# Kernel optimization log

Hardware: AMD Instinct MI355X
Metric: run time of the kernel (lower is better)

The kernel has to match this reference:

```python
import jax, jax.numpy as jnp
import numpy as np

B, T, C = 4, 1024, 1024
H = 16
DH = C // H  # 64


def setup_inputs() -> dict:
    key = jax.random.key(0)
    ks = jax.random.split(key, 10)
    s = 0.02
    return {
        "x": jax.random.normal(ks[0], (B, T, C), dtype=jnp.float32),
        "Wq": jax.random.normal(ks[1], (C, C), dtype=jnp.float32) * s,
        "bq": jnp.zeros((C,), dtype=jnp.float32),
        "Wk": jax.random.normal(ks[2], (C, C), dtype=jnp.float32) * s,
        "bk": jnp.zeros((C,), dtype=jnp.float32),
        "Wv": jax.random.normal(ks[3], (C, C), dtype=jnp.float32) * s,
        "bv": jnp.zeros((C,), dtype=jnp.float32),
        "Wp": jax.random.normal(ks[4], (C, C), dtype=jnp.float32) * s,
        "bp": jnp.zeros((C,), dtype=jnp.float32),
    }


def reference(x, Wq, bq, Wk, bk, Wv, bv, Wp, bp):
    b, t, c = x.shape
    # QKV projections, split into heads: [b, H, t, DH]
    def heads(y):
        return y.reshape(b, t, H, DH).transpose(0, 2, 1, 3)
    q = heads(x @ Wq + bq)
    k = heads(x @ Wk + bk)
    v = heads(x @ Wv + bv)
    # Causal attention. Original masks with -inf BEFORE scaling; -inf*scale is
    # still -inf, so mask-then-scale == scale-then-mask.
    scores = jnp.einsum("bhqd,bhkd->bhqk", q, k) * (DH ** -0.5)
    causal = jnp.tril(jnp.ones((t, t), dtype=bool))
    scores = jnp.where(causal, scores, -jnp.inf)
    attn = jax.nn.softmax(scores, axis=-1)  # dropout p=0.0 -> identity
    ctx = jnp.einsum("bhqk,bhkd->bhqd", attn, v)
    ctx = ctx.transpose(0, 2, 1, 3).reshape(b, t, c)
    return ctx @ Wp + bp
```

## Files before the change

kernel.cpp:

```cpp
#include <hip/hip_runtime.h>


typedef unsigned short ushort_t;
typedef __attribute__((ext_vector_type(8))) __bf16 bf16x8;
typedef __attribute__((ext_vector_type(8))) unsigned short us8;
typedef __attribute__((ext_vector_type(4))) unsigned short us4;
typedef __attribute__((ext_vector_type(4))) float f32x4;

#define AS1 __attribute__((address_space(1)))
#define AS3 __attribute__((address_space(3)))

#define QSCALE 0.18033688011112042f

__device__ __forceinline__ ushort_t f2bf(float f) {
  unsigned int u = __float_as_uint(f);
  u += 0x7fffu + ((u >> 16) & 1u);
  return (ushort_t)(u >> 16);
}

__device__ __forceinline__ ushort_t f2bf_hw(float f) {
  union { __bf16 b; ushort_t u; } cv;
  cv.b = (__bf16)f;
  return cv.u;
}


__global__ void cvt_fused_kernel(const float* __restrict__ x,
                                 const float* __restrict__ Wq, const float* __restrict__ Wk,
                                 const float* __restrict__ Wv, const float* __restrict__ Wp,
                                 ushort_t* __restrict__ XB,
                                 ushort_t* __restrict__ WQKVT, ushort_t* __restrict__ WPT) {
  const int tid = threadIdx.x;
  if (blockIdx.x < 4096) {
    const int i = blockIdx.x * 256 + tid;
    const float4 v = reinterpret_cast<const float4*>(x)[i];
    us4 o;
    o.x = f2bf(v.x); o.y = f2bf(v.y); o.z = f2bf(v.z); o.w = f2bf(v.w);
    reinterpret_cast<us4*>(XB)[i] = o;
    return;
  }
  __shared__ float t[32][33];
  const int tt = blockIdx.x - 4096;
  const int z = tt >> 10;
  const int tile = tt & 1023;
  const int n0 = (tile & 31) * 32, k0 = (tile >> 5) * 32;
  const float* W = (z == 0) ? Wq : (z == 1) ? Wk : (z == 2) ? Wv : Wp;
  ushort_t* Wt = (z == 3) ? WPT : (WQKVT + ((size_t)z << 20));
  const float wscale = (z == 0) ? QSCALE : 1.0f;
  const int tx = tid & 31, ty = tid >> 5;
#pragma unroll
  for (int i = ty; i < 32; i += 8)
    t[i][tx] = W[(size_t)(k0 + i) * 1024 + n0 + tx];
  __syncthreads();
#pragma unroll
  for (int i = ty; i < 32; i += 8)
    Wt[(size_t)(n0 + i) * 1024 + k0 + tx] = f2bf(t[tx][i] * wscale);
}


__global__ __launch_bounds__(256, 3) void gemm_qkv128_kernel(
    const ushort_t* __restrict__ A, const ushort_t* __restrict__ Bt,
    const float* __restrict__ bq, const float* __restrict__ bk,
    const float* __restrict__ bv, ushort_t* __restrict__ QKVB,
    ushort_t* __restrict__ VT) {
  __shared__ ushort_t As[128 * 64];
  __shared__ ushort_t Bs[128 * 64];
  const int tid = threadIdx.x;
  const int wave = tid >> 6, lane = tid & 63;
  const int lgrp = lane >> 4, lmod = lane & 15;
  const int wr = wave >> 1, wc = wave & 1;
  const int swz = (blockIdx.x & 7) * 96 + (blockIdx.x >> 3);
  const int rowt = swz / 24, colt = swz % 24;
  const int row0 = rowt * 128, col0 = colt * 128;
  const bool isV = (colt >= 16);

  const int sslot = (tid & 7) ^ ((tid >> 3) & 7);
  const int srow = tid >> 3;

  auto stage = [&](int t) {
    const ushort_t* Asrc = A + (size_t)row0 * 1024 + t * 64 + sslot * 8;
    const ushort_t* Bsrc = Bt + (size_t)col0 * 1024 + t * 64 + sslot * 8;
#pragma unroll
    for (int i = 0; i < 4; ++i) {
      __builtin_amdgcn_global_load_lds(
          (AS1 void*)(Asrc + (size_t)(i * 32 + srow) * 1024),
          (AS3 void*)(As + (i * 256 + wave * 64) * 8), 16, 0, 0);
      __builtin_amdgcn_global_load_lds(
          (AS1 void*)(Bsrc + (size_t)(i * 32 + srow) * 1024),
          (AS3 void*)(Bs + (i * 256 + wave * 64) * 8), 16, 0, 0);
    }
  };

  f32x4 acc[4][4] = {};
  const int xm = lmod & 7;

  for (int t = 0; t < 16; ++t) {
    stage(t);
    asm volatile("s_waitcnt vmcnt(0)" ::: "memory");
    __builtin_amdgcn_s_barrier();

    bf16x8 af[4][2], bfr[4][2];
#pragma unroll
    for (int mi = 0; mi < 4; ++mi)
#pragma unroll
      for (int ks = 0; ks < 2; ++ks)
        af[mi][ks] = *reinterpret_cast<const bf16x8*>(
            &As[(wr * 64 + mi * 16 + lmod) * 64 + (((ks << 2) | lgrp) ^ xm) * 8]);
#pragma unroll
    for (int ni = 0; ni < 4; ++ni)
#pragma unroll
      for (int ks = 0; ks < 2; ++ks)
        bfr[ni][ks] = *reinterpret_cast<const bf16x8*>(
            &Bs[(wc * 64 + ni * 16 + lmod) * 64 + (((ks << 2) | lgrp) ^ xm) * 8]);

    __builtin_amdgcn_s_setprio(1);
#pragma unroll
    for (int mi = 0; mi < 4; ++mi)
#pragma unroll
      for (int ni = 0; ni < 4; ++ni)
#pragma unroll
        for (int ks = 0; ks < 2; ++ks)
          acc[mi][ni] = __builtin_amdgcn_mfma_f32_16x16x32_bf16(
              af[mi][ks], bfr[ni][ks], acc[mi][ni], 0, 0, 0);
    __builtin_amdgcn_s_setprio(0);
    __builtin_amdgcn_s_barrier();
  }

  if (!isV) {
    const float* bsel = (col0 < 1024) ? bq : bk;
    const float bsc = (col0 < 1024) ? QSCALE : 1.0f;
    float bvv[4];
#pragma unroll
    for (int ni = 0; ni < 4; ++ni)
      bvv[ni] = bsel[(col0 & 1023) + wc * 64 + ni * 16 + lmod] * bsc;
#pragma unroll
    for (int mi = 0; mi < 4; ++mi) {
#pragma unroll
      for (int ni = 0; ni < 4; ++ni) {
        const int col = col0 + wc * 64 + ni * 16 + lmod;
#pragma unroll
        for (int r = 0; r < 4; ++r) {
          const int row = row0 + wr * 64 + mi * 16 + lgrp * 4 + r;
          QKVB[(size_t)row * 3072 + col] = f2bf(acc[mi][ni][r] + bvv[ni]);
        }
      }
    }
  } else {
    float bvv[4];
#pragma unroll
    for (int ni = 0; ni < 4; ++ni)
      bvv[ni] = bv[(col0 - 2048) + wc * 64 + ni * 16 + lmod];
#pragma unroll
    for (int mi = 0; mi < 4; ++mi) {
#pragma unroll
      for (int ni = 0; ni < 4; ++ni) {
        const int hd = (col0 - 2048) + wc * 64 + ni * 16 + lmod;
        const int R = row0 + wr * 64 + mi * 16 + lgrp * 4;
        const int bb = R >> 10, tl = R & 1023;
        us4 o;
#pragma unroll
        for (int r = 0; r < 4; ++r) o[r] = f2bf(acc[mi][ni][r] + bvv[ni]);
        *reinterpret_cast<us4*>(VT + ((size_t)(bb * 16 + (hd >> 6)) * 64 + (hd & 63)) * 1024 + tl) = o;
      }
    }
  }
}


__global__ __launch_bounds__(256, 2) void gemm_proj_kernel(
    const ushort_t* __restrict__ A, const ushort_t* __restrict__ Bt,
    const float* __restrict__ bias, float* __restrict__ Cout) {
  __shared__ ushort_t As[64 * 64];
  __shared__ ushort_t Bs[128 * 64];
  const int tid = threadIdx.x;
  const int wave = tid >> 6, lane = tid & 63;
  const int lgrp = lane >> 4, lmod = lane & 15;
  const int wr = wave >> 1, wc = wave & 1;
  const int swz = (blockIdx.x & 7) * 64 + (blockIdx.x >> 3);
  const int row0 = (swz >> 3) * 64, col0 = (swz & 7) * 128;

  const int sslot = (tid & 7) ^ ((tid >> 3) & 7);
  const int srow = tid >> 3;

  auto stage = [&](int t) {
    const ushort_t* Asrc = A + (size_t)row0 * 1024 + t * 64 + sslot * 8;
    const ushort_t* Bsrc = Bt + (size_t)col0 * 1024 + t * 64 + sslot * 8;
#pragma unroll
    for (int i = 0; i < 2; ++i)
      __builtin_amdgcn_global_load_lds(
          (AS1 void*)(Asrc + (size_t)(i * 32 + srow) * 1024),
          (AS3 void*)(As + (i * 256 + wave * 64) * 8), 16, 0, 0);
#pragma unroll
    for (int i = 0; i < 4; ++i)
      __builtin_amdgcn_global_load_lds(
          (AS1 void*)(Bsrc + (size_t)(i * 32 + srow) * 1024),
          (AS3 void*)(Bs + (i * 256 + wave * 64) * 8), 16, 0, 0);
  };

  f32x4 acc[2][4] = {};
  const int xm = lmod & 7;

  for (int t = 0; t < 16; ++t) {
    stage(t);
    asm volatile("s_waitcnt vmcnt(0)" ::: "memory");
    __builtin_amdgcn_s_barrier();

    bf16x8 af[2][2], bfr[4][2];
#pragma unroll
    for (int mi = 0; mi < 2; ++mi)
#pragma unroll
      for (int ks = 0; ks < 2; ++ks)
        af[mi][ks] = *reinterpret_cast<const bf16x8*>(
            &As[(wr * 32 + mi * 16 + lmod) * 64 + (((ks << 2) | lgrp) ^ xm) * 8]);
#pragma unroll
    for (int ni = 0; ni < 4; ++ni)
#pragma unroll
      for (int ks = 0; ks < 2; ++ks)
        bfr[ni][ks] = *reinterpret_cast<const bf16x8*>(
            &Bs[(wc * 64 + ni * 16 + lmod) * 64 + (((ks << 2) | lgrp) ^ xm) * 8]);

    __builtin_amdgcn_s_setprio(1);
#pragma unroll
    for (int mi = 0; mi < 2; ++mi)
#pragma unroll
      for (int ni = 0; ni < 4; ++ni)
#pragma unroll
        for (int ks = 0; ks < 2; ++ks)
          acc[mi][ni] = __builtin_amdgcn_mfma_f32_16x16x32_bf16(
              af[mi][ks], bfr[ni][ks], acc[mi][ni], 0, 0, 0);
    __builtin_amdgcn_s_setprio(0);
    __builtin_amdgcn_s_barrier();
  }

  float bvv[4];
#pragma unroll
  for (int ni = 0; ni < 4; ++ni) bvv[ni] = bias[col0 + wc * 64 + ni * 16 + lmod];
#pragma unroll
  for (int mi = 0; mi < 2; ++mi)
#pragma unroll
    for (int ni = 0; ni < 4; ++ni) {
      const int col = col0 + wc * 64 + ni * 16 + lmod;
#pragma unroll
      for (int r = 0; r < 4; ++r) {
        const int row = row0 + wr * 32 + mi * 16 + lgrp * 4 + r;
        Cout[(size_t)row * 1024 + col] = acc[mi][ni][r] + bvv[ni];
      }
    }
}


__global__ __launch_bounds__(256, 2) void attn_kernel(
    const ushort_t* __restrict__ QKV, const ushort_t* __restrict__ VT,
    ushort_t* __restrict__ Og) {
  const int bid = blockIdx.x;
  const int swz = (bid & 7) * 64 + (bid >> 3);
  const int p = swz & 7, bh = swz >> 3;
  const int b = bh >> 4, h = bh & 15;
  const int jmax = 15 - p;
  const int tid = threadIdx.x;
  const int wave = tid >> 6, lane = tid & 63;
  const int lgrp = lane >> 4, lmod = lane & 15;

  __shared__ ushort_t Ks[64 * 72];
  __shared__ ushort_t Vs[64 * 72];
  __shared__ ushort_t Ps[4][2][16 * 72];

  const size_t xrow0 = (size_t)b * 1024;
  const int qlo = p * 64 + wave * 16;
  const int qhi = jmax * 64 + wave * 16;

  bf16x8 qfl[2], qfh[2];
#pragma unroll
  for (int ks = 0; ks < 2; ++ks) {
    qfl[ks] = *reinterpret_cast<const bf16x8*>(
        QKV + (xrow0 + qlo + lmod) * 3072 + h * 64 + ks * 32 + lgrp * 8);
    qfh[ks] = *reinterpret_cast<const bf16x8*>(
        QKV + (xrow0 + qhi + lmod) * 3072 + h * 64 + ks * 32 + lgrp * 8);
  }

  f32x4 ol[4] = {}, oh[4] = {};
  float ll[4] = {0.f, 0.f, 0.f, 0.f}, lh[4] = {0.f, 0.f, 0.f, 0.f};

  const int sr = tid >> 3;
  const int scc = (tid & 7) << 3;
  us8 kreg0, kreg1, vreg0, vreg1;

  auto load_tile = [&](int j) {
    const ushort_t* kp = QKV + (xrow0 + j * 64 + sr) * 3072 + 1024 + h * 64 + scc;
    kreg0 = *reinterpret_cast<const us8*>(kp);
    kreg1 = *reinterpret_cast<const us8*>(kp + 32 * 3072);
    const ushort_t* vp = VT + ((size_t)bh * 64 + sr) * 1024 + j * 64 + scc;
    vreg0 = *reinterpret_cast<const us8*>(vp);
    vreg1 = *reinterpret_cast<const us8*>(vp + 32 * 1024);
  };
  auto write_tile = [&]() {
    *reinterpret_cast<us8*>(&Ks[sr * 72 + scc]) = kreg0;
    *reinterpret_cast<us8*>(&Ks[(32 + sr) * 72 + scc]) = kreg1;
    *reinterpret_cast<us8*>(&Vs[sr * 72 + scc]) = vreg0;
    *reinterpret_cast<us8*>(&Vs[(32 + sr) * 72 + scc]) = vreg1;
  };

  auto mask_diag = [&](f32x4* s) {
    const int qloc = wave * 16 + lgrp * 4;
#pragma unroll
    for (int cg = 0; cg < 4; ++cg) {
      const int kcol = cg * 16 + lmod;
#pragma unroll
      for (int r = 0; r < 4; ++r)
        if (kcol > qloc + r) s[cg][r] = -1e30f;
    }
  };

  auto step = [&](const bf16x8* qf, f32x4* oacc, float* lsum, bool diag) {
    f32x4 s[4];
    __builtin_amdgcn_s_setprio(1);
#pragma unroll
    for (int cg = 0; cg < 4; ++cg) {
      f32x4 a = {};
#pragma unroll
      for (int ks = 0; ks < 2; ++ks) {
        bf16x8 kf = *reinterpret_cast<const bf16x8*>(
            &Ks[(cg * 16 + lmod) * 72 + ks * 32 + lgrp * 8]);
        a = __builtin_amdgcn_mfma_f32_16x16x32_bf16(qf[ks], kf, a, 0, 0, 0);
      }
      s[cg] = a;
    }
    __builtin_amdgcn_s_setprio(0);
    if (diag) mask_diag(s);
#pragma unroll
    for (int cg = 0; cg < 4; ++cg)
#pragma unroll
      for (int r = 0; r < 4; ++r) s[cg][r] = exp2f(s[cg][r]);
#pragma unroll
    for (int r = 0; r < 4; ++r)
      lsum[r] += (s[0][r] + s[1][r]) + (s[2][r] + s[3][r]);
#pragma unroll
    for (int cg = 0; cg < 4; ++cg)
#pragma unroll
      for (int r = 0; r < 4; ++r)
        Ps[wave][1][(lgrp * 4 + r) * 72 + cg * 16 + lmod] = f2bf_hw(s[cg][r]);
    __builtin_amdgcn_s_setprio(1);
#pragma unroll
    for (int ks = 0; ks < 2; ++ks) {
      bf16x8 pf = *reinterpret_cast<const bf16x8*>(
          &Ps[wave][1][lmod * 72 + ks * 32 + lgrp * 8]);
#pragma unroll
      for (int dhg = 0; dhg < 4; ++dhg) {
        bf16x8 vf = *reinterpret_cast<const bf16x8*>(
            &Vs[(dhg * 16 + lmod) * 72 + ks * 32 + lgrp * 8]);
        oacc[dhg] = __builtin_amdgcn_mfma_f32_16x16x32_bf16(pf, vf, oacc[dhg], 0, 0, 0);
      }
    }
    __builtin_amdgcn_s_setprio(0);
  };

  auto step_dual = [&](bool diag_lo) {
    f32x4 sl[4], sh[4];
    __builtin_amdgcn_s_setprio(1);
#pragma unroll
    for (int cg = 0; cg < 4; ++cg) {
      f32x4 al = {}, ah = {};
#pragma unroll
      for (int ks = 0; ks < 2; ++ks) {
        bf16x8 kf = *reinterpret_cast<const bf16x8*>(
            &Ks[(cg * 16 + lmod) * 72 + ks * 32 + lgrp * 8]);
        al = __builtin_amdgcn_mfma_f32_16x16x32_bf16(qfl[ks], kf, al, 0, 0, 0);
        ah = __builtin_amdgcn_mfma_f32_16x16x32_bf16(qfh[ks], kf, ah, 0, 0, 0);
      }
      sl[cg] = al; sh[cg] = ah;
    }
    __builtin_amdgcn_s_setprio(0);
    if (diag_lo) mask_diag(sl);
#pragma unroll
    for (int cg = 0; cg < 4; ++cg)
#pragma unroll
      for (int r = 0; r < 4; ++r) {
        sl[cg][r] = exp2f(sl[cg][r]);
        sh[cg][r] = exp2f(sh[cg][r]);
      }
#pragma unroll
    for (int r = 0; r < 4; ++r) {
      ll[r] += (sl[0][r] + sl[1][r]) + (sl[2][r] + sl[3][r]);
      lh[r] += (sh[0][r] + sh[1][r]) + (sh[2][r] + sh[3][r]);
    }
#pragma unroll
    for (int cg = 0; cg < 4; ++cg)
#pragma unroll
      for (int r = 0; r < 4; ++r) {
        Ps[wave][0][(lgrp * 4 + r) * 72 + cg * 16 + lmod] = f2bf_hw(sl[cg][r]);
        Ps[wave][1][(lgrp * 4 + r) * 72 + cg * 16 + lmod] = f2bf_hw(sh[cg][r]);
      }
    __builtin_amdgcn_s_setprio(1);
#pragma unroll
    for (int ks = 0; ks < 2; ++ks) {
      bf16x8 pfl = *reinterpret_cast<const bf16x8*>(
          &Ps[wave][0][lmod * 72 + ks * 32 + lgrp * 8]);
      bf16x8 pfh = *reinterpret_cast<const bf16x8*>(
          &Ps[wave][1][lmod * 72 + ks * 32 + lgrp * 8]);
#pragma unroll
      for (int dhg = 0; dhg < 4; ++dhg) {
        bf16x8 vf = *reinterpret_cast<const bf16x8*>(
            &Vs[(dhg * 16 + lmod) * 72 + ks * 32 + lgrp * 8]);
        ol[dhg] = __builtin_amdgcn_mfma_f32_16x16x32_bf16(pfl, vf, ol[dhg], 0, 0, 0);
        oh[dhg] = __builtin_amdgcn_mfma_f32_16x16x32_bf16(pfh, vf, oh[dhg], 0, 0, 0);
      }
    }
    __builtin_amdgcn_s_setprio(0);
  };

  load_tile(0);
  for (int j = 0; j <= jmax; ++j) {
    __syncthreads();
    write_tile();
    __syncthreads();
    if (j < jmax) load_tile(j + 1);
    if (j <= p) step_dual(j == p);
    else step(qfh, oh, lh, j == jmax);
  }

#pragma unroll
  for (int m = 1; m <= 8; m <<= 1)
#pragma unroll
    for (int r = 0; r < 4; ++r) {
      ll[r] += __shfl_xor(ll[r], m);
      lh[r] += __shfl_xor(lh[r], m);
    }

#pragma unroll
  for (int dhg = 0; dhg < 4; ++dhg) {
    const int col = h * 64 + dhg * 16 + lmod;
#pragma unroll
    for (int r = 0; r < 4; ++r) {
      Og[(xrow0 + qlo + lgrp * 4 + r) * 1024 + col] = f2bf_hw(ol[dhg][r] / ll[r]);
      Og[(xrow0 + qhi + lgrp * 4 + r) * 1024 + col] = f2bf_hw(oh[dhg][r] / lh[r]);
    }
  }
}


extern "C" void kernel_launch(void* const* d_in, const int* in_sizes, int n_in,
                              void* d_out, int out_size, void* d_ws, size_t ws_size,
                              hipStream_t stream) {
  const float* x  = (const float*)d_in[0];
  const float* Wq = (const float*)d_in[1];
  const float* bq = (const float*)d_in[2];
  const float* Wk = (const float*)d_in[3];
  const float* bk = (const float*)d_in[4];
  const float* Wv = (const float*)d_in[5];
  const float* bv = (const float*)d_in[6];
  const float* Wp = (const float*)d_in[7];
  const float* bp = (const float*)d_in[8];
  float* out = (float*)d_out;

  char* ws = (char*)d_ws;
  ushort_t* XB    = (ushort_t*)(ws);
  ushort_t* WQKVT = (ushort_t*)(ws + ( 8ull << 20));
  ushort_t* WPT   = (ushort_t*)(ws + (14ull << 20));
  ushort_t* QKVB  = (ushort_t*)(ws + (16ull << 20));
  ushort_t* VT    = (ushort_t*)(ws + (40ull << 20));

  cvt_fused_kernel<<<8192, 256, 0, stream>>>(x, Wq, Wk, Wv, Wp, XB, WQKVT, WPT);
  gemm_qkv128_kernel<<<768, 256, 0, stream>>>(XB, WQKVT, bq, bk, bv, QKVB, VT);
  attn_kernel<<<512, 256, 0, stream>>>(QKVB, VT, XB);
  gemm_proj_kernel<<<512, 256, 0, stream>>>(XB, WPT, bp, out);
}
```

Baseline: 86.38 us.

## Split paired causal query tiles into separate blocks for more parallelism

The attention kernel previously processed two query tiles per block (a low tile and its mirrored high tile) so that every block did the same causal work, sharing each loaded K/V tile between them. Now each block handles one 64-row query tile, with a launch of 1024 blocks and block indices interleaving short and long tiles, and occupancy is raised to 4 blocks per CU. This aims at more parallelism and lower register and LDS pressure, but each K/V tile is loaded once per query tile rather than once per pair, and block runtimes become unequal.

Measured after the change: 97.75 us. +13.2%, slower.

```diff
diff --git a/kernel.cpp b/kernel.cpp
--- a/kernel.cpp
+++ b/kernel.cpp
@@ -249,37 +249,33 @@
 }
 
 
-__global__ __launch_bounds__(256, 2) void attn_kernel(
+__global__ __launch_bounds__(256, 4) void attn_kernel(
     const ushort_t* __restrict__ QKV, const ushort_t* __restrict__ VT,
     ushort_t* __restrict__ Og) {
   const int bid = blockIdx.x;
-  const int swz = (bid & 7) * 64 + (bid >> 3);
-  const int p = swz & 7, bh = swz >> 3;
+  const int swz = (bid & 7) * 128 + (bid >> 3);
+  const int pslot = swz & 15, bh = swz >> 4;
+  const int p = (pslot & 1) ? (15 - (pslot >> 1)) : (pslot >> 1);
   const int b = bh >> 4, h = bh & 15;
-  const int jmax = 15 - p;
   const int tid = threadIdx.x;
   const int wave = tid >> 6, lane = tid & 63;
   const int lgrp = lane >> 4, lmod = lane & 15;
 
   __shared__ ushort_t Ks[64 * 72];
   __shared__ ushort_t Vs[64 * 72];
-  __shared__ ushort_t Ps[4][2][16 * 72];
+  __shared__ ushort_t Ps[4][16 * 72];
 
   const size_t xrow0 = (size_t)b * 1024;
-  const int qlo = p * 64 + wave * 16;
-  const int qhi = jmax * 64 + wave * 16;
-
-  bf16x8 qfl[2], qfh[2];
-#pragma unroll
-  for (int ks = 0; ks < 2; ++ks) {
-    qfl[ks] = *reinterpret_cast<const bf16x8*>(
-        QKV + (xrow0 + qlo + lmod) * 3072 + h * 64 + ks * 32 + lgrp * 8);
-    qfh[ks] = *reinterpret_cast<const bf16x8*>(
-        QKV + (xrow0 + qhi + lmod) * 3072 + h * 64 + ks * 32 + lgrp * 8);
-  }
-
-  f32x4 ol[4] = {}, oh[4] = {};
-  float ll[4] = {0.f, 0.f, 0.f, 0.f}, lh[4] = {0.f, 0.f, 0.f, 0.f};
+  const int qr0 = p * 64 + wave * 16;
+
+  bf16x8 qf[2];
+#pragma unroll
+  for (int ks = 0; ks < 2; ++ks)
+    qf[ks] = *reinterpret_cast<const bf16x8*>(
+        QKV + (xrow0 + qr0 + lmod) * 3072 + h * 64 + ks * 32 + lgrp * 8);
+
+  f32x4 oacc[4] = {};
+  float lsum[4] = {0.f, 0.f, 0.f, 0.f};
 
   const int sr = tid >> 3;
   const int scc = (tid & 7) << 3;
@@ -300,18 +296,13 @@
     *reinterpret_cast<us8*>(&Vs[(32 + sr) * 72 + scc]) = vreg1;
   };
 
-  auto mask_diag = [&](f32x4* s) {
-    const int qloc = wave * 16 + lgrp * 4;
-#pragma unroll
-    for (int cg = 0; cg < 4; ++cg) {
-      const int kcol = cg * 16 + lmod;
-#pragma unroll
-      for (int r = 0; r < 4; ++r)
-        if (kcol > qloc + r) s[cg][r] = -1e30f;
-    }
-  };
-
-  auto step = [&](const bf16x8* qf, f32x4* oacc, float* lsum, bool diag) {
+  for (int j = 0; j <= p; ++j) {
+    if (j == 0) load_tile(0);
+    __syncthreads();
+    write_tile();
+    __syncthreads();
+    if (j < p) load_tile(j + 1);
+
     f32x4 s[4];
     __builtin_amdgcn_s_setprio(1);
 #pragma unroll
@@ -326,7 +317,18 @@
       s[cg] = a;
     }
     __builtin_amdgcn_s_setprio(0);
-    if (diag) mask_diag(s);
+
+    if (j == p) {
+      const int qloc = wave * 16 + lgrp * 4;
+#pragma unroll
+      for (int cg = 0; cg < 4; ++cg) {
+        const int kcol = cg * 16 + lmod;
+#pragma unroll
+        for (int r = 0; r < 4; ++r)
+          if (kcol > qloc + r) s[cg][r] = -1e30f;
+      }
+    }
+
 #pragma unroll
     for (int cg = 0; cg < 4; ++cg)
 #pragma unroll
@@ -338,12 +340,13 @@
     for (int cg = 0; cg < 4; ++cg)
 #pragma unroll
       for (int r = 0; r < 4; ++r)
-        Ps[wave][1][(lgrp * 4 + r) * 72 + cg * 16 + lmod] = f2bf_hw(s[cg][r]);
+        Ps[wave][(lgrp * 4 + r) * 72 + cg * 16 + lmod] = f2bf_hw(s[cg][r]);
+
     __builtin_amdgcn_s_setprio(1);
 #pragma unroll
     for (int ks = 0; ks < 2; ++ks) {
       bf16x8 pf = *reinterpret_cast<const bf16x8*>(
-          &Ps[wave][1][lmod * 72 + ks * 32 + lgrp * 8]);
+          &Ps[wave][lmod * 72 + ks * 32 + lgrp * 8]);
 #pragma unroll
       for (int dhg = 0; dhg < 4; ++dhg) {
         bf16x8 vf = *reinterpret_cast<const bf16x8*>(
@@ -352,88 +355,19 @@
       }
     }
     __builtin_amdgcn_s_setprio(0);
-  };
-
-  auto step_dual = [&](bool diag_lo) {
-    f32x4 sl[4], sh[4];
-    __builtin_amdgcn_s_setprio(1);
-#pragma unroll
-    for (int cg = 0; cg < 4; ++cg) {
-      f32x4 al = {}, ah = {};
-#pragma unroll
-      for (int ks = 0; ks < 2; ++ks) {
-        bf16x8 kf = *reinterpret_cast<const bf16x8*>(
-            &Ks[(cg * 16 + lmod) * 72 + ks * 32 + lgrp * 8]);
-        al = __builtin_amdgcn_mfma_f32_16x16x32_bf16(qfl[ks], kf, al, 0, 0, 0);
-        ah = __builtin_amdgcn_mfma_f32_16x16x32_bf16(qfh[ks], kf, ah, 0, 0, 0);
-      }
-      sl[cg] = al; sh[cg] = ah;
-    }
-    __builtin_amdgcn_s_setprio(0);
-    if (diag_lo) mask_diag(sl);
-#pragma unroll
-    for (int cg = 0; cg < 4; ++cg)
-#pragma unroll
-      for (int r = 0; r < 4; ++r) {
-        sl[cg][r] = exp2f(sl[cg][r]);
-        sh[cg][r] = exp2f(sh[cg][r]);
-      }
-#pragma unroll
-    for (int r = 0; r < 4; ++r) {
-      ll[r] += (sl[0][r] + sl[1][r]) + (sl[2][r] + sl[3][r]);
-      lh[r] += (sh[0][r] + sh[1][r]) + (sh[2][r] + sh[3][r]);
-    }
-#pragma unroll
-    for (int cg = 0; cg < 4; ++cg)
-#pragma unroll
-      for (int r = 0; r < 4; ++r) {
-        Ps[wave][0][(lgrp * 4 + r) * 72 + cg * 16 + lmod] = f2bf_hw(sl[cg][r]);
-        Ps[wave][1][(lgrp * 4 + r) * 72 + cg * 16 + lmod] = f2bf_hw(sh[cg][r]);
-      }
-    __builtin_amdgcn_s_setprio(1);
-#pragma unroll
-    for (int ks = 0; ks < 2; ++ks) {
-      bf16x8 pfl = *reinterpret_cast<const bf16x8*>(
-          &Ps[wave][0][lmod * 72 + ks * 32 + lgrp * 8]);
-      bf16x8 pfh = *reinterpret_cast<const bf16x8*>(
-          &Ps[wave][1][lmod * 72 + ks * 32 + lgrp * 8]);
-#pragma unroll
-      for (int dhg = 0; dhg < 4; ++dhg) {
-        bf16x8 vf = *reinterpret_cast<const bf16x8*>(
-            &Vs[(dhg * 16 + lmod) * 72 + ks * 32 + lgrp * 8]);
-        ol[dhg] = __builtin_amdgcn_mfma_f32_16x16x32_bf16(pfl, vf, ol[dhg], 0, 0, 0);
-        oh[dhg] = __builtin_amdgcn_mfma_f32_16x16x32_bf16(pfh, vf, oh[dhg], 0, 0, 0);
-      }
-    }
-    __builtin_amdgcn_s_setprio(0);
-  };
-
-  load_tile(0);
-  for (int j = 0; j <= jmax; ++j) {
-    __syncthreads();
-    write_tile();
-    __syncthreads();
-    if (j < jmax) load_tile(j + 1);
-    if (j <= p) step_dual(j == p);
-    else step(qfh, oh, lh, j == jmax);
   }
 
 #pragma unroll
   for (int m = 1; m <= 8; m <<= 1)
 #pragma unroll
-    for (int r = 0; r < 4; ++r) {
-      ll[r] += __shfl_xor(ll[r], m);
-      lh[r] += __shfl_xor(lh[r], m);
-    }
+    for (int r = 0; r < 4; ++r) lsum[r] += __shfl_xor(lsum[r], m);
 
 #pragma unroll
   for (int dhg = 0; dhg < 4; ++dhg) {
     const int col = h * 64 + dhg * 16 + lmod;
 #pragma unroll
-    for (int r = 0; r < 4; ++r) {
-      Og[(xrow0 + qlo + lgrp * 4 + r) * 1024 + col] = f2bf_hw(ol[dhg][r] / ll[r]);
-      Og[(xrow0 + qhi + lgrp * 4 + r) * 1024 + col] = f2bf_hw(oh[dhg][r] / lh[r]);
-    }
+    for (int r = 0; r < 4; ++r)
+      Og[(xrow0 + qr0 + lgrp * 4 + r) * 1024 + col] = f2bf_hw(oacc[dhg][r] / lsum[r]);
   }
 }
 
@@ -461,6 +395,6 @@
 
   cvt_fused_kernel<<<8192, 256, 0, stream>>>(x, Wq, Wk, Wv, Wp, XB, WQKVT, WPT);
   gemm_qkv128_kernel<<<768, 256, 0, stream>>>(XB, WQKVT, bq, bk, bv, QKVB, VT);
-  attn_kernel<<<512, 256, 0, stream>>>(QKVB, VT, XB);
+  attn_kernel<<<1024, 256, 0, stream>>>(QKVB, VT, XB);
   gemm_proj_kernel<<<512, 256, 0, stream>>>(XB, WPT, bp, out);
 }
```
